# Kernel tuning notes

Measured on AMD Instinct MI355X. Metric: run time of the kernel, lower is better.

Reference implementation:

```python
import jax, jax.numpy as jnp
import numpy as np

N = 50000   # nodes
E = 600000  # directed edges (avg degree ~12)
F_IN = 128
HID = 128
N_LAYERS = 7


def setup_inputs() -> dict:
    key = jax.random.key(0)
    ks = jax.random.split(key, 5)
    x = jax.random.normal(ks[0], (N, F_IN), dtype=jnp.float32)
    edge_index = jax.random.randint(ks[1], (2, E), 0, N, dtype=jnp.int64)
    Ws = jax.random.normal(ks[2], (N_LAYERS, F_IN, HID), dtype=jnp.float32) * 0.05
    bs = jnp.zeros((N_LAYERS, HID), dtype=jnp.float32)
    lin_w = jax.random.normal(ks[3], (HID, 1), dtype=jnp.float32) * 0.05
    lin_b = jnp.zeros((1,), dtype=jnp.float32)
    return {"x": x, "edge_index": edge_index, "Ws": Ws, "bs": bs,
            "lin_w": lin_w, "lin_b": lin_b}


def reference(x, edge_index, Ws, bs, lin_w, lin_b):
    n = x.shape[0]
    loop = jnp.arange(n, dtype=edge_index.dtype)
    # PyG GCNConv default: add self-loops, symmetric normalization.
    src = jnp.concatenate([edge_index[0], loop])  # [E+N] message sources (j)
    dst = jnp.concatenate([edge_index[1], loop])  # [E+N] message targets (i)
    deg = jax.ops.segment_sum(jnp.ones_like(dst, dtype=x.dtype), dst, num_segments=n)
    dis = jnp.where(deg > 0, jax.lax.rsqrt(deg), 0.0)  # deg^-1/2, 0 for isolated
    norm = dis[src] * dis[dst]                          # [E+N]

    def gcn_layer(h, W, b):
        h = h @ W                                        # linear first (as in PyG)
        msg = h[src] * norm[:, None]                     # gather + scale
        return jax.ops.segment_sum(msg, dst, num_segments=n) + b

    h = x
    for i in range(N_LAYERS):
        h = jax.nn.relu(gcn_layer(h, Ws[i], bs[i]))
    out = h @ lin_w + lin_b                              # [N, 1]
    return out.squeeze()                                 # [N]
```

## Files before the change

### kernel.cpp

```cpp
#include <hip/hip_runtime.h>

#define HID 128
#define ASPITCH 132
#define BM 64


__global__ __launch_bounds__(256) void k_count(const int* __restrict__ ei, int E,
                                               int* __restrict__ deg) {
    int e = blockIdx.x * 256 + threadIdx.x;
    if (e < E) atomicAdd(&deg[ei[E + e]], 1);
}

__global__ __launch_bounds__(256) void k_scan1(const int* __restrict__ deg,
                                               int* __restrict__ rowptr,
                                               int* __restrict__ partial, int n) {
    __shared__ int s[256];
    int tid = threadIdx.x;
    int i = blockIdx.x * 256 + tid;
    int v = (i < n) ? deg[i] : 0;
    s[tid] = v;
    __syncthreads();
    for (int off = 1; off < 256; off <<= 1) {
        int t = (tid >= off) ? s[tid - off] : 0;
        __syncthreads();
        s[tid] += t;
        __syncthreads();
    }
    if (i < n) rowptr[i] = s[tid] - v;
    if (tid == 255) partial[blockIdx.x] = s[255];
}

__global__ __launch_bounds__(256) void k_scan2(int* __restrict__ partial, int nb) {
    __shared__ int s[256];
    int tid = threadIdx.x;
    int v = (tid < nb) ? partial[tid] : 0;
    s[tid] = v;
    __syncthreads();
    for (int off = 1; off < 256; off <<= 1) {
        int t = (tid >= off) ? s[tid - off] : 0;
        __syncthreads();
        s[tid] += t;
        __syncthreads();
    }
    if (tid < nb) partial[tid] = s[tid] - v;
}

__global__ __launch_bounds__(256) void k_scan3(int* __restrict__ rowptr,
                                               const int* __restrict__ partial,
                                               int n, int E) {
    int i = blockIdx.x * 256 + threadIdx.x;
    if (i < n) rowptr[i] += partial[blockIdx.x];
    if (i == 0) rowptr[n] = E;
}

__global__ __launch_bounds__(256) void k_dis(const int* __restrict__ deg,
                                             float* __restrict__ dis, int n) {
    int i = blockIdx.x * 256 + threadIdx.x;
    if (i < n) dis[i] = 1.0f / sqrtf((float)(deg[i] + 1));
}

__global__ __launch_bounds__(256) void k_fill(const int* __restrict__ ei, int E,
                                              const int* __restrict__ rowptr,
                                              int* __restrict__ cursor,
                                              int* __restrict__ col) {
    int e = blockIdx.x * 256 + threadIdx.x;
    if (e < E) {
        int d = ei[E + e];
        int p = atomicAdd(&cursor[d], 1);
        col[rowptr[d] + p] = ei[e];
    }
}


__global__ __launch_bounds__(256, 3) void k_gemm0(const float* __restrict__ A,
                                                  const float* __restrict__ W,
                                                  const float* __restrict__ dis,
                                                  float* __restrict__ T, int n) {
    __shared__ float As[BM * ASPITCH];
    int r0 = blockIdx.x * BM;
    int tid = threadIdx.x;
    int rows = n - r0; if (rows > BM) rows = BM;
    {
        const float4* A4 = (const float4*)(A + (size_t)r0 * HID);
        int tot = rows * (HID / 4);
        for (int i = tid; i < tot; i += 256) {
            int row = i >> 5, c = (i & 31) << 2;
            *(float4*)&As[row * ASPITCH + c] = A4[i];
        }
    }
    __syncthreads();

    int tx = tid & 31, ty = tid >> 5;
    int rr0 = ty * 8;
    const float4* W4 = (const float4*)W;

    float acc[8][4];
    #pragma unroll
    for (int r = 0; r < 8; ++r) { acc[r][0]=0.f; acc[r][1]=0.f; acc[r][2]=0.f; acc[r][3]=0.f; }

    float4 wa0 = W4[0 * 32 + tx];
    float4 wa1 = W4[1 * 32 + tx];
    float4 wa2 = W4[2 * 32 + tx];
    float4 wa3 = W4[3 * 32 + tx];
    float4 wb0, wb1, wb2, wb3;

    #pragma unroll 1
    for (int k = 0; k < HID; k += 8) {
        wb0 = W4[(k + 4) * 32 + tx];
        wb1 = W4[(k + 5) * 32 + tx];
        wb2 = W4[(k + 6) * 32 + tx];
        wb3 = W4[(k + 7) * 32 + tx];
        #pragma unroll
        for (int r = 0; r < 8; ++r) {
            float4 a = *(const float4*)&As[(rr0 + r) * ASPITCH + k];
            acc[r][0] = fmaf(a.x, wa0.x, acc[r][0]);
            acc[r][1] = fmaf(a.x, wa0.y, acc[r][1]);
            acc[r][2] = fmaf(a.x, wa0.z, acc[r][2]);
            acc[r][3] = fmaf(a.x, wa0.w, acc[r][3]);
            acc[r][0] = fmaf(a.y, wa1.x, acc[r][0]);
            acc[r][1] = fmaf(a.y, wa1.y, acc[r][1]);
            acc[r][2] = fmaf(a.y, wa1.z, acc[r][2]);
            acc[r][3] = fmaf(a.y, wa1.w, acc[r][3]);
            acc[r][0] = fmaf(a.z, wa2.x, acc[r][0]);
            acc[r][1] = fmaf(a.z, wa2.y, acc[r][1]);
            acc[r][2] = fmaf(a.z, wa2.z, acc[r][2]);
            acc[r][3] = fmaf(a.z, wa2.w, acc[r][3]);
            acc[r][0] = fmaf(a.w, wa3.x, acc[r][0]);
            acc[r][1] = fmaf(a.w, wa3.y, acc[r][1]);
            acc[r][2] = fmaf(a.w, wa3.z, acc[r][2]);
            acc[r][3] = fmaf(a.w, wa3.w, acc[r][3]);
        }
        if (k + 8 < HID) {
            wa0 = W4[(k + 8)  * 32 + tx];
            wa1 = W4[(k + 9)  * 32 + tx];
            wa2 = W4[(k + 10) * 32 + tx];
            wa3 = W4[(k + 11) * 32 + tx];
        }
        #pragma unroll
        for (int r = 0; r < 8; ++r) {
            float4 a = *(const float4*)&As[(rr0 + r) * ASPITCH + k + 4];
            acc[r][0] = fmaf(a.x, wb0.x, acc[r][0]);
            acc[r][1] = fmaf(a.x, wb0.y, acc[r][1]);
            acc[r][2] = fmaf(a.x, wb0.z, acc[r][2]);
            acc[r][3] = fmaf(a.x, wb0.w, acc[r][3]);
            acc[r][0] = fmaf(a.y, wb1.x, acc[r][0]);
            acc[r][1] = fmaf(a.y, wb1.y, acc[r][1]);
            acc[r][2] = fmaf(a.y, wb1.z, acc[r][2]);
            acc[r][3] = fmaf(a.y, wb1.w, acc[r][3]);
            acc[r][0] = fmaf(a.z, wb2.x, acc[r][0]);
            acc[r][1] = fmaf(a.z, wb2.y, acc[r][1]);
            acc[r][2] = fmaf(a.z, wb2.z, acc[r][2]);
            acc[r][3] = fmaf(a.z, wb2.w, acc[r][3]);
            acc[r][0] = fmaf(a.w, wb3.x, acc[r][0]);
            acc[r][1] = fmaf(a.w, wb3.y, acc[r][1]);
            acc[r][2] = fmaf(a.w, wb3.z, acc[r][2]);
            acc[r][3] = fmaf(a.w, wb3.w, acc[r][3]);
        }
    }

    int c0 = tx * 4;
    #pragma unroll
    for (int r = 0; r < 8; ++r) {
        int row = rr0 + r;
        if (row < rows) {
            float d = dis[r0 + row];
            float4 o = make_float4(acc[r][0] * d, acc[r][1] * d, acc[r][2] * d, acc[r][3] * d);
            *(float4*)&T[(size_t)(r0 + row) * HID + c0] = o;
        }
    }
}

__global__ __launch_bounds__(256, 3) void k_aggemm(const float* __restrict__ Uin,
                                                   const float* __restrict__ W,
                                                   const float* __restrict__ b,
                                                   const float* __restrict__ dis,
                                                   const int* __restrict__ rowptr,
                                                   const int* __restrict__ col,
                                                   float* __restrict__ Uout, int n) {
    __shared__ float S[BM * HID];
    int r0 = blockIdx.x * BM;
    int tid = threadIdx.x;
    int hw = tid >> 5, lane = tid & 31;
    size_t foff = (size_t)(lane * 4);
    float4 bb = *(const float4*)&b[lane * 4];
    const float4* W4 = (const float4*)W;
    int c0 = lane * 4;

    #pragma unroll 1
    for (int chunk = 0; chunk < 2; ++chunk) {
        int rbase = hw * 8 + chunk * 4;

        #pragma unroll 1
        for (int rr = 0; rr < 4; ++rr) {
            int row = r0 + rbase + rr;
            float4 acc = make_float4(0.f, 0.f, 0.f, 0.f);
            if (row < n) {
                acc = *(const float4*)&Uin[(size_t)row * HID + foff];
                float4 acc2 = make_float4(0.f, 0.f, 0.f, 0.f);
                int e = rowptr[row], e1 = rowptr[row + 1];
                for (; e + 8 <= e1; e += 8) {
                    int j0 = col[e + 0];
                    int j1 = col[e + 1];
                    int j2 = col[e + 2];
                    int j3 = col[e + 3];
                    int j4 = col[e + 4];
                    int j5 = col[e + 5];
                    int j6 = col[e + 6];
                    int j7 = col[e + 7];
                    float4 v0 = *(const float4*)&Uin[(size_t)j0 * HID + foff];
                    float4 v1 = *(const float4*)&Uin[(size_t)j1 * HID + foff];
                    float4 v2 = *(const float4*)&Uin[(size_t)j2 * HID + foff];
                    float4 v3 = *(const float4*)&Uin[(size_t)j3 * HID + foff];
                    float4 v4 = *(const float4*)&Uin[(size_t)j4 * HID + foff];
                    float4 v5 = *(const float4*)&Uin[(size_t)j5 * HID + foff];
                    float4 v6 = *(const float4*)&Uin[(size_t)j6 * HID + foff];
                    float4 v7 = *(const float4*)&Uin[(size_t)j7 * HID + foff];
                    acc.x  += (v0.x + v1.x) + (v2.x + v3.x);
                    acc.y  += (v0.y + v1.y) + (v2.y + v3.y);
                    acc.z  += (v0.z + v1.z) + (v2.z + v3.z);
                    acc.w  += (v0.w + v1.w) + (v2.w + v3.w);
                    acc2.x += (v4.x + v5.x) + (v6.x + v7.x);
                    acc2.y += (v4.y + v5.y) + (v6.y + v7.y);
                    acc2.z += (v4.z + v5.z) + (v6.z + v7.z);
                    acc2.w += (v4.w + v5.w) + (v6.w + v7.w);
                }
                for (; e + 2 <= e1; e += 2) {
                    int j0 = col[e + 0];
                    int j1 = col[e + 1];
                    float4 v0 = *(const float4*)&Uin[(size_t)j0 * HID + foff];
                    float4 v1 = *(const float4*)&Uin[(size_t)j1 * HID + foff];
                    acc.x  += v0.x; acc.y  += v0.y; acc.z  += v0.z; acc.w  += v0.w;
                    acc2.x += v1.x; acc2.y += v1.y; acc2.z += v1.z; acc2.w += v1.w;
                }
                if (e < e1) {
                    int j = col[e];
                    float4 v = *(const float4*)&Uin[(size_t)j * HID + foff];
                    acc.x += v.x; acc.y += v.y; acc.z += v.z; acc.w += v.w;
                }
                float d = dis[row];
                acc.x = fmaxf(fmaf(d, acc.x + acc2.x, bb.x), 0.0f);
                acc.y = fmaxf(fmaf(d, acc.y + acc2.y, bb.y), 0.0f);
                acc.z = fmaxf(fmaf(d, acc.z + acc2.z, bb.z), 0.0f);
                acc.w = fmaxf(fmaf(d, acc.w + acc2.w, bb.w), 0.0f);
            }
            *(float4*)&S[(rbase + rr) * HID + lane * 4] = acc;
        }

        float acc[4][4];
        #pragma unroll
        for (int r = 0; r < 4; ++r) { acc[r][0]=0.f; acc[r][1]=0.f; acc[r][2]=0.f; acc[r][3]=0.f; }

        float4 wa0 = W4[0 * 32 + lane];
        float4 wa1 = W4[1 * 32 + lane];
        float4 wa2 = W4[2 * 32 + lane];
        float4 wa3 = W4[3 * 32 + lane];
        float4 wb0, wb1, wb2, wb3;

        #pragma unroll 1
        for (int k = 0; k < HID; k += 8) {
            wb0 = W4[(k + 4) * 32 + lane];
            wb1 = W4[(k + 5) * 32 + lane];
            wb2 = W4[(k + 6) * 32 + lane];
            wb3 = W4[(k + 7) * 32 + lane];
            #pragma unroll
            for (int r = 0; r < 4; ++r) {
                float4 a = *(const float4*)&S[(rbase + r) * HID + k];
                acc[r][0] = fmaf(a.x, wa0.x, acc[r][0]);
                acc[r][1] = fmaf(a.x, wa0.y, acc[r][1]);
                acc[r][2] = fmaf(a.x, wa0.z, acc[r][2]);
                acc[r][3] = fmaf(a.x, wa0.w, acc[r][3]);
                acc[r][0] = fmaf(a.y, wa1.x, acc[r][0]);
                acc[r][1] = fmaf(a.y, wa1.y, acc[r][1]);
                acc[r][2] = fmaf(a.y, wa1.z, acc[r][2]);
                acc[r][3] = fmaf(a.y, wa1.w, acc[r][3]);
                acc[r][0] = fmaf(a.z, wa2.x, acc[r][0]);
                acc[r][1] = fmaf(a.z, wa2.y, acc[r][1]);
                acc[r][2] = fmaf(a.z, wa2.z, acc[r][2]);
                acc[r][3] = fmaf(a.z, wa2.w, acc[r][3]);
                acc[r][0] = fmaf(a.w, wa3.x, acc[r][0]);
                acc[r][1] = fmaf(a.w, wa3.y, acc[r][1]);
                acc[r][2] = fmaf(a.w, wa3.z, acc[r][2]);
                acc[r][3] = fmaf(a.w, wa3.w, acc[r][3]);
            }
            if (k + 8 < HID) {
                wa0 = W4[(k + 8)  * 32 + lane];
                wa1 = W4[(k + 9)  * 32 + lane];
                wa2 = W4[(k + 10) * 32 + lane];
                wa3 = W4[(k + 11) * 32 + lane];
            }
            #pragma unroll
            for (int r = 0; r < 4; ++r) {
                float4 a = *(const float4*)&S[(rbase + r) * HID + k + 4];
                acc[r][0] = fmaf(a.x, wb0.x, acc[r][0]);
                acc[r][1] = fmaf(a.x, wb0.y, acc[r][1]);
                acc[r][2] = fmaf(a.x, wb0.z, acc[r][2]);
                acc[r][3] = fmaf(a.x, wb0.w, acc[r][3]);
                acc[r][0] = fmaf(a.y, wb1.x, acc[r][0]);
                acc[r][1] = fmaf(a.y, wb1.y, acc[r][1]);
                acc[r][2] = fmaf(a.y, wb1.z, acc[r][2]);
                acc[r][3] = fmaf(a.y, wb1.w, acc[r][3]);
                acc[r][0] = fmaf(a.z, wb2.x, acc[r][0]);
                acc[r][1] = fmaf(a.z, wb2.y, acc[r][1]);
                acc[r][2] = fmaf(a.z, wb2.z, acc[r][2]);
                acc[r][3] = fmaf(a.z, wb2.w, acc[r][3]);
                acc[r][0] = fmaf(a.w, wb3.x, acc[r][0]);
                acc[r][1] = fmaf(a.w, wb3.y, acc[r][1]);
                acc[r][2] = fmaf(a.w, wb3.z, acc[r][2]);
                acc[r][3] = fmaf(a.w, wb3.w, acc[r][3]);
            }
        }

        #pragma unroll
        for (int r = 0; r < 4; ++r) {
            int row = r0 + rbase + r;
            if (row < n) {
                float d = dis[row];
                float4 o = make_float4(acc[r][0] * d, acc[r][1] * d, acc[r][2] * d, acc[r][3] * d);
                *(float4*)&Uout[(size_t)row * HID + c0] = o;
            }
        }
    }
}

__global__ __launch_bounds__(256) void k_agglin(const float* __restrict__ Uin,
                                                const float* __restrict__ b,
                                                const float* __restrict__ dis,
                                                const int* __restrict__ rowptr,
                                                const int* __restrict__ col,
                                                const float* __restrict__ lw,
                                                const float* __restrict__ lb,
                                                float* __restrict__ out, int n) {
    int node = (blockIdx.x * 256 + threadIdx.x) >> 5;
    int lane = threadIdx.x & 31;
    if (node >= n) return;
    size_t foff = (size_t)(lane * 4);
    float4 acc = *(const float4*)&Uin[(size_t)node * HID + foff];
    float4 acc2 = make_float4(0.f, 0.f, 0.f, 0.f);
    int e = rowptr[node], e1 = rowptr[node + 1];
    for (; e + 8 <= e1; e += 8) {
        int j0 = col[e + 0];
        int j1 = col[e + 1];
        int j2 = col[e + 2];
        int j3 = col[e + 3];
        int j4 = col[e + 4];
        int j5 = col[e + 5];
        int j6 = col[e + 6];
        int j7 = col[e + 7];
        float4 v0 = *(const float4*)&Uin[(size_t)j0 * HID + foff];
        float4 v1 = *(const float4*)&Uin[(size_t)j1 * HID + foff];
        float4 v2 = *(const float4*)&Uin[(size_t)j2 * HID + foff];
        float4 v3 = *(const float4*)&Uin[(size_t)j3 * HID + foff];
        float4 v4 = *(const float4*)&Uin[(size_t)j4 * HID + foff];
        float4 v5 = *(const float4*)&Uin[(size_t)j5 * HID + foff];
        float4 v6 = *(const float4*)&Uin[(size_t)j6 * HID + foff];
        float4 v7 = *(const float4*)&Uin[(size_t)j7 * HID + foff];
        acc.x  += (v0.x + v1.x) + (v2.x + v3.x);
        acc.y  += (v0.y + v1.y) + (v2.y + v3.y);
        acc.z  += (v0.z + v1.z) + (v2.z + v3.z);
        acc.w  += (v0.w + v1.w) + (v2.w + v3.w);
        acc2.x += (v4.x + v5.x) + (v6.x + v7.x);
        acc2.y += (v4.y + v5.y) + (v6.y + v7.y);
        acc2.z += (v4.z + v5.z) + (v6.z + v7.z);
        acc2.w += (v4.w + v5.w) + (v6.w + v7.w);
    }
    for (; e + 2 <= e1; e += 2) {
        int j0 = col[e + 0];
        int j1 = col[e + 1];
        float4 v0 = *(const float4*)&Uin[(size_t)j0 * HID + foff];
        float4 v1 = *(const float4*)&Uin[(size_t)j1 * HID + foff];
        acc.x  += v0.x; acc.y  += v0.y; acc.z  += v0.z; acc.w  += v0.w;
        acc2.x += v1.x; acc2.y += v1.y; acc2.z += v1.z; acc2.w += v1.w;
    }
    if (e < e1) {
        int j = col[e];
        float4 v = *(const float4*)&Uin[(size_t)j * HID + foff];
        acc.x += v.x; acc.y += v.y; acc.z += v.z; acc.w += v.w;
    }
    float d = dis[node];
    float4 bb = *(const float4*)&b[lane * 4];
    float4 h;
    h.x = fmaxf(fmaf(d, acc.x + acc2.x, bb.x), 0.0f);
    h.y = fmaxf(fmaf(d, acc.y + acc2.y, bb.y), 0.0f);
    h.z = fmaxf(fmaf(d, acc.z + acc2.z, bb.z), 0.0f);
    h.w = fmaxf(fmaf(d, acc.w + acc2.w, bb.w), 0.0f);
    float4 ww = *(const float4*)&lw[lane * 4];
    float s = h.x * ww.x + h.y * ww.y + h.z * ww.z + h.w * ww.w;
    #pragma unroll
    for (int o = 16; o > 0; o >>= 1) s += __shfl_down(s, o, 64);
    if (lane == 0) out[node] = s + lb[0];
}


extern "C" void kernel_launch(void* const* d_in, const int* in_sizes, int n_in,
                              void* d_out, int out_size, void* d_ws, size_t ws_size,
                              hipStream_t stream) {
    const float* x     = (const float*)d_in[0];
    const int*   ei    = (const int*)d_in[1];
    const float* Ws    = (const float*)d_in[2];
    const float* bs    = (const float*)d_in[3];
    const float* lin_w = (const float*)d_in[4];
    const float* lin_b = (const float*)d_in[5];
    float* out = (float*)d_out;

    int n = in_sizes[0] / HID;
    int E = in_sizes[1] / 2;
    int L = in_sizes[2] / (HID * HID);

    char* ws = (char*)d_ws;
    size_t off = 0;
    auto alloc = [&](size_t bytes) -> void* {
        void* p = ws + off;
        off += (bytes + 255) & ~(size_t)255;
        return p;
    };
    int*   deg     = (int*)alloc((size_t)n * 4);
    int*   cursor  = (int*)alloc((size_t)n * 4);
    int*   rowptr  = (int*)alloc((size_t)(n + 1) * 4);
    int*   partial = (int*)alloc(1024);
    float* dis     = (float*)alloc((size_t)n * 4);
    int*   col     = (int*)alloc((size_t)E * 4);
    float* ubuf0   = (float*)alloc((size_t)n * HID * 4);
    float* ubuf1   = (float*)alloc((size_t)n * HID * 4);
    (void)ws_size;

    hipMemsetAsync(deg, 0, (size_t)n * 4, stream);
    hipMemsetAsync(cursor, 0, (size_t)n * 4, stream);

    int eb = (E + 255) / 256;
    int nb = (n + 255) / 256;
    k_count<<<eb, 256, 0, stream>>>(ei, E, deg);
    k_scan1<<<nb, 256, 0, stream>>>(deg, rowptr, partial, n);
    k_scan2<<<1, 256, 0, stream>>>(partial, nb);
    k_scan3<<<nb, 256, 0, stream>>>(rowptr, partial, n, E);
    k_dis<<<nb, 256, 0, stream>>>(deg, dis, n);
    k_fill<<<eb, 256, 0, stream>>>(ei, E, rowptr, cursor, col);

    int gb = (n + BM - 1) / BM;
    int hb = (n + 7) / 8;

    k_gemm0<<<gb, 256, 0, stream>>>(x, Ws, dis, ubuf0, n);

    float* uin = ubuf0;
    float* uout = ubuf1;
    for (int i = 0; i + 1 < L; ++i) {
        k_aggemm<<<gb, 256, 0, stream>>>(uin, Ws + (size_t)(i + 1) * HID * HID,
                                         bs + (size_t)i * HID, dis, rowptr, col,
                                         uout, n);
        float* t = uin; uin = uout; uout = t;
    }

    k_agglin<<<hb, 256, 0, stream>>>(uin, bs + (size_t)(L - 1) * HID, dis,
                                     rowptr, col, lin_w, lin_b, out, n);
}
```

Baseline: 591.9 us.

## Overlap neighbor gather of second tile with GEMM of first tile in aggemm

Each block now handles two 64-row tiles. After aggregating the first tile into shared memory, the GEMM k-loop for that tile is interleaved with masked 8-wide neighbor gathers for the second tile, so gather latency hides behind FMA work, followed by the second tile's GEMM. This doubles shared memory and accumulator registers (8 rows per warp), lowers the occupancy hint to 2 blocks, and halves the grid size, which risks less latency hiding and fewer waves overall.

```diff
diff --git a/kernel.cpp b/kernel.cpp
--- a/kernel.cpp
+++ b/kernel.cpp
@@ -170,101 +170,130 @@
     }
 }
 
-__global__ __launch_bounds__(256, 3) void k_aggemm(const float* __restrict__ Uin,
+__global__ __launch_bounds__(256, 2) void k_aggemm(const float* __restrict__ Uin,
                                                    const float* __restrict__ W,
                                                    const float* __restrict__ b,
                                                    const float* __restrict__ dis,
                                                    const int* __restrict__ rowptr,
                                                    const int* __restrict__ col,
                                                    float* __restrict__ Uout, int n) {
-    __shared__ float S[BM * HID];
-    int r0 = blockIdx.x * BM;
+    __shared__ float S0[BM * HID];
+    __shared__ float S1[BM * HID];
     int tid = threadIdx.x;
     int hw = tid >> 5, lane = tid & 31;
+    int t0 = blockIdx.x * (2 * BM);
+    int t1 = t0 + BM;
     size_t foff = (size_t)(lane * 4);
     float4 bb = *(const float4*)&b[lane * 4];
     const float4* W4 = (const float4*)W;
-    int c0 = lane * 4;
+    int rr0 = hw * 8;
 
     #pragma unroll 1
-    for (int chunk = 0; chunk < 2; ++chunk) {
-        int rbase = hw * 8 + chunk * 4;
-
+    for (int rr = 0; rr < 8; ++rr) {
+        int row = t0 + rr0 + rr;
+        float4 ga = make_float4(0.f, 0.f, 0.f, 0.f);
+        if (row < n) {
+            ga = *(const float4*)&Uin[(size_t)row * HID + foff];
+            float4 ga2 = make_float4(0.f, 0.f, 0.f, 0.f);
+            int e = rowptr[row], e1 = rowptr[row + 1];
+            for (; e + 8 <= e1; e += 8) {
+                int j0 = col[e + 0];
+                int j1 = col[e + 1];
+                int j2 = col[e + 2];
+                int j3 = col[e + 3];
+                int j4 = col[e + 4];
+                int j5 = col[e + 5];
+                int j6 = col[e + 6];
+                int j7 = col[e + 7];
+                float4 v0 = *(const float4*)&Uin[(size_t)j0 * HID + foff];
+                float4 v1 = *(const float4*)&Uin[(size_t)j1 * HID + foff];
+                float4 v2 = *(const float4*)&Uin[(size_t)j2 * HID + foff];
+                float4 v3 = *(const float4*)&Uin[(size_t)j3 * HID + foff];
+                float4 v4 = *(const float4*)&Uin[(size_t)j4 * HID + foff];
+                float4 v5 = *(const float4*)&Uin[(size_t)j5 * HID + foff];
+                float4 v6 = *(const float4*)&Uin[(size_t)j6 * HID + foff];
+                float4 v7 = *(const float4*)&Uin[(size_t)j7 * HID + foff];
+                ga.x  += (v0.x + v1.x) + (v2.x + v3.x);
+                ga.y  += (v0.y + v1.y) + (v2.y + v3.y);
+                ga.z  += (v0.z + v1.z) + (v2.z + v3.z);
+                ga.w  += (v0.w + v1.w) + (v2.w + v3.w);
+                ga2.x += (v4.x + v5.x) + (v6.x + v7.x);
+                ga2.y += (v4.y + v5.y) + (v6.y + v7.y);
+                ga2.z += (v4.z + v5.z) + (v6.z + v7.z);
+                ga2.w += (v4.w + v5.w) + (v6.w + v7.w);
+            }
+            for (; e + 2 <= e1; e += 2) {
+                int j0 = col[e + 0];
+                int j1 = col[e + 1];
+                float4 v0 = *(const float4*)&Uin[(size_t)j0 * HID + foff];
+                float4 v1 = *(const float4*)&Uin[(size_t)j1 * HID + foff];
+                ga.x  += v0.x; ga.y  += v0.y; ga.z  += v0.z; ga.w  += v0.w;
+                ga2.x += v1.x; ga2.y += v1.y; ga2.z += v1.z; ga2.w += v1.w;
+            }
+            if (e < e1) {
+                int j = col[e];
+                float4 v = *(const float4*)&Uin[(size_t)j * HID + foff];
+                ga.x += v.x; ga.y += v.y; ga.z += v.z; ga.w += v.w;
+            }
+            float d = dis[row];
+            ga.x = fmaxf(fmaf(d, ga.x + ga2.x, bb.x), 0.0f);
+            ga.y = fmaxf(fmaf(d, ga.y + ga2.y, bb.y), 0.0f);
+            ga.z = fmaxf(fmaf(d, ga.z + ga2.z, bb.z), 0.0f);
+            ga.w = fmaxf(fmaf(d, ga.w + ga2.w, bb.w), 0.0f);
+        }
+        *(float4*)&S0[(rr0 + rr) * HID + lane * 4] = ga;
+    }
+
+    float acc[8][4];
+    #pragma unroll
+    for (int r = 0; r < 8; ++r) { acc[r][0]=0.f; acc[r][1]=0.f; acc[r][2]=0.f; acc[r][3]=0.f; }
+
+    float4 wa0 = W4[0 * 32 + lane];
+    float4 wa1 = W4[1 * 32 + lane];
+    float4 wa2 = W4[2 * 32 + lane];
+    float4 wa3 = W4[3 * 32 + lane];
+    float4 wb0, wb1, wb2, wb3;
+    int k = 0;
+
+    #pragma unroll 1
+    for (int g = 0; g < 8; ++g) {
+        int grow = t1 + rr0 + g;
+        float4 ga = make_float4(0.f, 0.f, 0.f, 0.f);
+        float4 ga2 = make_float4(0.f, 0.f, 0.f, 0.f);
+        int ge = 0, ge1 = 0;
+        if (grow < n) {
+            ga = *(const float4*)&Uin[(size_t)grow * HID + foff];
+            ge = rowptr[grow]; ge1 = rowptr[grow + 1];
+        }
         #pragma unroll 1
-        for (int rr = 0; rr < 4; ++rr) {
-            int row = r0 + rbase + rr;
-            float4 acc = make_float4(0.f, 0.f, 0.f, 0.f);
-            if (row < n) {
-                acc = *(const float4*)&Uin[(size_t)row * HID + foff];
-                float4 acc2 = make_float4(0.f, 0.f, 0.f, 0.f);
-                int e = rowptr[row], e1 = rowptr[row + 1];
-                for (; e + 8 <= e1; e += 8) {
-                    int j0 = col[e + 0];
-                    int j1 = col[e + 1];
-                    int j2 = col[e + 2];
-                    int j3 = col[e + 3];
-                    int j4 = col[e + 4];
-                    int j5 = col[e + 5];
-                    int j6 = col[e + 6];
-                    int j7 = col[e + 7];
-                    float4 v0 = *(const float4*)&Uin[(size_t)j0 * HID + foff];
-                    float4 v1 = *(const float4*)&Uin[(size_t)j1 * HID + foff];
-                    float4 v2 = *(const float4*)&Uin[(size_t)j2 * HID + foff];
-                    float4 v3 = *(const float4*)&Uin[(size_t)j3 * HID + foff];
-                    float4 v4 = *(const float4*)&Uin[(size_t)j4 * HID + foff];
-                    float4 v5 = *(const float4*)&Uin[(size_t)j5 * HID + foff];
-                    float4 v6 = *(const float4*)&Uin[(size_t)j6 * HID + foff];
-                    float4 v7 = *(const float4*)&Uin[(size_t)j7 * HID + foff];
-                    acc.x  += (v0.x + v1.x) + (v2.x + v3.x);
-                    acc.y  += (v0.y + v1.y) + (v2.y + v3.y);
-                    acc.z  += (v0.z + v1.z) + (v2.z + v3.z);
-                    acc.w  += (v0.w + v1.w) + (v2.w + v3.w);
-                    acc2.x += (v4.x + v5.x) + (v6.x + v7.x);
-                    acc2.y += (v4.y + v5.y) + (v6.y + v7.y);
-                    acc2.z += (v4.z + v5.z) + (v6.z + v7.z);
-                    acc2.w += (v4.w + v5.w) + (v6.w + v7.w);
-                }
-                for (; e + 2 <= e1; e += 2) {
-                    int j0 = col[e + 0];
-                    int j1 = col[e + 1];
-                    float4 v0 = *(const float4*)&Uin[(size_t)j0 * HID + foff];
-                    float4 v1 = *(const float4*)&Uin[(size_t)j1 * HID + foff];
-                    acc.x  += v0.x; acc.y  += v0.y; acc.z  += v0.z; acc.w  += v0.w;
-                    acc2.x += v1.x; acc2.y += v1.y; acc2.z += v1.z; acc2.w += v1.w;
-                }
-                if (e < e1) {
-                    int j = col[e];
-                    float4 v = *(const float4*)&Uin[(size_t)j * HID + foff];
-                    acc.x += v.x; acc.y += v.y; acc.z += v.z; acc.w += v.w;
-                }
-                float d = dis[row];
-                acc.x = fmaxf(fmaf(d, acc.x + acc2.x, bb.x), 0.0f);
-                acc.y = fmaxf(fmaf(d, acc.y + acc2.y, bb.y), 0.0f);
-                acc.z = fmaxf(fmaf(d, acc.z + acc2.z, bb.z), 0.0f);
-                acc.w = fmaxf(fmaf(d, acc.w + acc2.w, bb.w), 0.0f);
-            }
-            *(float4*)&S[(rbase + rr) * HID + lane * 4] = acc;
-        }
-
-        float acc[4][4];
-        #pragma unroll
-        for (int r = 0; r < 4; ++r) { acc[r][0]=0.f; acc[r][1]=0.f; acc[r][2]=0.f; acc[r][3]=0.f; }
-
-        float4 wa0 = W4[0 * 32 + lane];
-        float4 wa1 = W4[1 * 32 + lane];
-        float4 wa2 = W4[2 * 32 + lane];
-        float4 wa3 = W4[3 * 32 + lane];
-        float4 wb0, wb1, wb2, wb3;
-
-        #pragma unroll 1
-        for (int k = 0; k < HID; k += 8) {
+        for (int s = 0; s < 2; ++s) {
+            bool m0 = ge + 0 < ge1, m1 = ge + 1 < ge1, m2 = ge + 2 < ge1, m3 = ge + 3 < ge1;
+            bool m4 = ge + 4 < ge1, m5 = ge + 5 < ge1, m6 = ge + 6 < ge1, m7 = ge + 7 < ge1;
+            int j0 = col[m0 ? ge + 0 : 0];
+            int j1 = col[m1 ? ge + 1 : 0];
+            int j2 = col[m2 ? ge + 2 : 0];
+            int j3 = col[m3 ? ge + 3 : 0];
+            int j4 = col[m4 ? ge + 4 : 0];
+            int j5 = col[m5 ? ge + 5 : 0];
+            int j6 = col[m6 ? ge + 6 : 0];
+            int j7 = col[m7 ? ge + 7 : 0];
+            float4 v0 = *(const float4*)&Uin[(size_t)j0 * HID + foff];
+            float4 v1 = *(const float4*)&Uin[(size_t)j1 * HID + foff];
+            float4 v2 = *(const float4*)&Uin[(size_t)j2 * HID + foff];
+            float4 v3 = *(const float4*)&Uin[(size_t)j3 * HID + foff];
+            float4 v4 = *(const float4*)&Uin[(size_t)j4 * HID + foff];
+            float4 v5 = *(const float4*)&Uin[(size_t)j5 * HID + foff];
+            float4 v6 = *(const float4*)&Uin[(size_t)j6 * HID + foff];
+            float4 v7 = *(const float4*)&Uin[(size_t)j7 * HID + foff];
+            ge = (ge + 8 < ge1) ? ge + 8 : ge1;
+
             wb0 = W4[(k + 4) * 32 + lane];
             wb1 = W4[(k + 5) * 32 + lane];
             wb2 = W4[(k + 6) * 32 + lane];
             wb3 = W4[(k + 7) * 32 + lane];
             #pragma unroll
-            for (int r = 0; r < 4; ++r) {
-                float4 a = *(const float4*)&S[(rbase + r) * HID + k];
+            for (int r = 0; r < 8; ++r) {
+                float4 a = *(const float4*)&S0[(rr0 + r) * HID + k];
                 acc[r][0] = fmaf(a.x, wa0.x, acc[r][0]);
                 acc[r][1] = fmaf(a.x, wa0.y, acc[r][1]);
                 acc[r][2] = fmaf(a.x, wa0.z, acc[r][2]);
@@ -289,8 +318,8 @@
                 wa3 = W4[(k + 11) * 32 + lane];
             }
             #pragma unroll
-            for (int r = 0; r < 4; ++r) {
-                float4 a = *(const float4*)&S[(rbase + r) * HID + k + 4];
+            for (int r = 0; r < 8; ++r) {
+                float4 a = *(const float4*)&S0[(rr0 + r) * HID + k + 4];
                 acc[r][0] = fmaf(a.x, wb0.x, acc[r][0]);
                 acc[r][1] = fmaf(a.x, wb0.y, acc[r][1]);
                 acc[r][2] = fmaf(a.x, wb0.z, acc[r][2]);
@@ -308,14 +337,123 @@
                 acc[r][2] = fmaf(a.w, wb3.z, acc[r][2]);
                 acc[r][3] = fmaf(a.w, wb3.w, acc[r][3]);
             }
-        }
-
+            k += 8;
+
+            float4 w0_ = m0 ? v0 : make_float4(0.f,0.f,0.f,0.f);
+            float4 w1_ = m1 ? v1 : make_float4(0.f,0.f,0.f,0.f);
+            float4 w2_ = m2 ? v2 : make_float4(0.f,0.f,0.f,0.f);
+            float4 w3_ = m3 ? v3 : make_float4(0.f,0.f,0.f,0.f);
+            float4 w4_ = m4 ? v4 : make_float4(0.f,0.f,0.f,0.f);
+            float4 w5_ = m5 ? v5 : make_float4(0.f,0.f,0.f,0.f);
+            float4 w6_ = m6 ? v6 : make_float4(0.f,0.f,0.f,0.f);
+            float4 w7_ = m7 ? v7 : make_float4(0.f,0.f,0.f,0.f);
+            ga.x  += (w0_.x + w1_.x) + (w2_.x + w3_.x);
+            ga.y  += (w0_.y + w1_.y) + (w2_.y + w3_.y);
+            ga.z  += (w0_.z + w1_.z) + (w2_.z + w3_.z);
+            ga.w  += (w0_.w + w1_.w) + (w2_.w + w3_.w);
+            ga2.x += (w4_.x + w5_.x) + (w6_.x + w7_.x);
+            ga2.y += (w4_.y + w5_.y) + (w6_.y + w7_.y);
+            ga2.z += (w4_.z + w5_.z) + (w6_.z + w7_.z);
+            ga2.w += (w4_.w + w5_.w) + (w6_.w + w7_.w);
+        }
+        for (; ge < ge1; ++ge) {
+            int j = col[ge];
+            float4 v = *(const float4*)&Uin[(size_t)j * HID + foff];
+            ga.x += v.x; ga.y += v.y; ga.z += v.z; ga.w += v.w;
+        }
+        float4 hv = make_float4(0.f, 0.f, 0.f, 0.f);
+        if (grow < n) {
+            float d = dis[grow];
+            hv.x = fmaxf(fmaf(d, ga.x + ga2.x, bb.x), 0.0f);
+            hv.y = fmaxf(fmaf(d, ga.y + ga2.y, bb.y), 0.0f);
+            hv.z = fmaxf(fmaf(d, ga.z + ga2.z, bb.z), 0.0f);
+            hv.w = fmaxf(fmaf(d, ga.w + ga2.w, bb.w), 0.0f);
+        }
+        *(float4*)&S1[(rr0 + g) * HID + lane * 4] = hv;
+    }
+
+    {
+        int c0 = lane * 4;
         #pragma unroll
-        for (int r = 0; r < 4; ++r) {
-            int row = r0 + rbase + r;
+        for (int r = 0; r < 8; ++r) {
+            int row = t0 + rr0 + r;
             if (row < n) {
                 float d = dis[row];
-                float4 o = make_float4(acc[r][0] * d, acc[r][1] * d, acc[r][2] * d, acc[r][3] * d);
+                float4 o = make_float4(acc[r][0]*d, acc[r][1]*d, acc[r][2]*d, acc[r][3]*d);
+                *(float4*)&Uout[(size_t)row * HID + c0] = o;
+            }
+        }
+    }
+
+    #pragma unroll
+    for (int r = 0; r < 8; ++r) { acc[r][0]=0.f; acc[r][1]=0.f; acc[r][2]=0.f; acc[r][3]=0.f; }
+    wa0 = W4[0 * 32 + lane];
+    wa1 = W4[1 * 32 + lane];
+    wa2 = W4[2 * 32 + lane];
+    wa3 = W4[3 * 32 + lane];
+
+    #pragma unroll 1
+    for (int kk = 0; kk < HID; kk += 8) {
+        wb0 = W4[(kk + 4) * 32 + lane];
+        wb1 = W4[(kk + 5) * 32 + lane];
+        wb2 = W4[(kk + 6) * 32 + lane];
+        wb3 = W4[(kk + 7) * 32 + lane];
+        #pragma unroll
+        for (int r = 0; r < 8; ++r) {
+            float4 a = *(const float4*)&S1[(rr0 + r) * HID + kk];
+            acc[r][0] = fmaf(a.x, wa0.x, acc[r][0]);
+            acc[r][1] = fmaf(a.x, wa0.y, acc[r][1]);
+            acc[r][2] = fmaf(a.x, wa0.z, acc[r][2]);
+            acc[r][3] = fmaf(a.x, wa0.w, acc[r][3]);
+            acc[r][0] = fmaf(a.y, wa1.x, acc[r][0]);
+            acc[r][1] = fmaf(a.y, wa1.y, acc[r][1]);
+            acc[r][2] = fmaf(a.y, wa1.z, acc[r][2]);
+            acc[r][3] = fmaf(a.y, wa1.w, acc[r][3]);
+            acc[r][0] = fmaf(a.z, wa2.x, acc[r][0]);
+            acc[r][1] = fmaf(a.z, wa2.y, acc[r][1]);
+            acc[r][2] = fmaf(a.z, wa2.z, acc[r][2]);
+            acc[r][3] = fmaf(a.z, wa2.w, acc[r][3]);
+            acc[r][0] = fmaf(a.w, wa3.x, acc[r][0]);
+            acc[r][1] = fmaf(a.w, wa3.y, acc[r][1]);
+            acc[r][2] = fmaf(a.w, wa3.z, acc[r][2]);
+            acc[r][3] = fmaf(a.w, wa3.w, acc[r][3]);
+        }
+        if (kk + 8 < HID) {
+            wa0 = W4[(kk + 8)  * 32 + lane];
+            wa1 = W4[(kk + 9)  * 32 + lane];
+            wa2 = W4[(kk + 10) * 32 + lane];
+            wa3 = W4[(kk + 11) * 32 + lane];
+        }
+        #pragma unroll
+        for (int r = 0; r < 8; ++r) {
+            float4 a = *(const float4*)&S1[(rr0 + r) * HID + kk + 4];
+            acc[r][0] = fmaf(a.x, wb0.x, acc[r][0]);
+            acc[r][1] = fmaf(a.x, wb0.y, acc[r][1]);
+            acc[r][2] = fmaf(a.x, wb0.z, acc[r][2]);
+            acc[r][3] = fmaf(a.x, wb0.w, acc[r][3]);
+            acc[r][0] = fmaf(a.y, wb1.x, acc[r][0]);
+            acc[r][1] = fmaf(a.y, wb1.y, acc[r][1]);
+            acc[r][2] = fmaf(a.y, wb1.z, acc[r][2]);
+            acc[r][3] = fmaf(a.y, wb1.w, acc[r][3]);
+            acc[r][0] = fmaf(a.z, wb2.x, acc[r][0]);
+            acc[r][1] = fmaf(a.z, wb2.y, acc[r][1]);
+            acc[r][2] = fmaf(a.z, wb2.z, acc[r][2]);
+            acc[r][3] = fmaf(a.z, wb2.w, acc[r][3]);
+            acc[r][0] = fmaf(a.w, wb3.x, acc[r][0]);
+            acc[r][1] = fmaf(a.w, wb3.y, acc[r][1]);
+            acc[r][2] = fmaf(a.w, wb3.z, acc[r][2]);
+            acc[r][3] = fmaf(a.w, wb3.w, acc[r][3]);
+        }
+    }
+
+    {
+        int c0 = lane * 4;
+        #pragma unroll
+        for (int r = 0; r < 8; ++r) {
+            int row = t1 + rr0 + r;
+            if (row < n) {
+                float d = dis[row];
+                float4 o = make_float4(acc[r][0]*d, acc[r][1]*d, acc[r][2]*d, acc[r][3]*d);
                 *(float4*)&Uout[(size_t)row * HID + c0] = o;
             }
         }
@@ -435,10 +573,11 @@
     k_dis<<<nb, 256, 0, stream>>>(deg, dis, n);
     k_fill<<<eb, 256, 0, stream>>>(ei, E, rowptr, cursor, col);
 
-    int gb = (n + BM - 1) / BM;
-    int hb = (n + 7) / 8;
-
-    k_gemm0<<<gb, 256, 0, stream>>>(x, Ws, dis, ubuf0, n);
+    int gb0 = (n + BM - 1) / BM;
+    int gb  = (n + 2 * BM - 1) / (2 * BM);
+    int hb  = (n + 7) / 8;
+
+    k_gemm0<<<gb0, 256, 0, stream>>>(x, Ws, dis, ubuf0, n);
 
     float* uin = ubuf0;
     float* uout = ubuf1;
```

After: 645.3 us. +9.0%, slower.
